# Kernel optimization log

Measured on AMD Instinct MI355X. Metric: run time of the kernel, lower is better.

The kernel has to match this reference:

```python
import jax, jax.numpy as jnp
import numpy as np

N_NODE = 118
DM, DP, DR, DH, DN, DPHI, DE = 768, 128, 128, 256, 256, 192, 256
N_OUT = 2
NEG = -1e9

leaky = lambda z: jnp.where(z >= 0, z, 0.01 * z)


def lstm_layer(x_seq, W_ih, W_hh, b_ih, b_hh):
    # x_seq: [B, T, in]; W_ih: [4H, in]; W_hh: [4H, H]; gate order i,f,g,o (torch)
    B = x_seq.shape[0]
    H = W_hh.shape[1]

    def step(carry, xt):
        h, c = carry
        gates = xt @ W_ih.T + h @ W_hh.T + b_ih + b_hh  # [B, 4H]
        i, f, g, o = jnp.split(gates, 4, axis=1)
        c = jax.nn.sigmoid(f) * c + jax.nn.sigmoid(i) * jnp.tanh(g)
        h = jax.nn.sigmoid(o) * jnp.tanh(c)
        return (h, c), h

    h0 = jnp.zeros((B, H), x_seq.dtype)
    (_, _), hs = jax.lax.scan(step, (h0, h0), jnp.swapaxes(x_seq, 0, 1))
    return jnp.swapaxes(hs, 0, 1)  # [B, T, H]


def setup_inputs() -> dict:
    key = jax.random.key(0)
    ks = jax.random.split(key, 32)
    n_feat, T = 128, 2048
    sc = 0.05
    inp = {}
    inp["x"] = jax.random.normal(ks[0], (N_NODE, T, n_feat), jnp.float32)
    h_pmt = jax.random.uniform(ks[1], (N_NODE, 2), jnp.float32)
    act = jax.random.randint(ks[2], (N_NODE, 1), 0, 2).astype(jnp.float32)
    inp["x_tag"] = jnp.concatenate([h_pmt, act], axis=1)
    # LSTM params (2 layers, hidden=DP)
    inp["W_ih0"] = jax.random.normal(ks[3], (4 * DP, n_feat), jnp.float32) * sc
    inp["W_hh0"] = jax.random.normal(ks[4], (4 * DP, DP), jnp.float32) * sc
    inp["b_ih0"] = jnp.zeros((4 * DP,), jnp.float32)
    inp["b_hh0"] = jnp.zeros((4 * DP,), jnp.float32)
    inp["W_ih1"] = jax.random.normal(ks[5], (4 * DP, DP), jnp.float32) * sc
    inp["W_hh1"] = jax.random.normal(ks[6], (4 * DP, DP), jnp.float32) * sc
    inp["b_ih1"] = jnp.zeros((4 * DP,), jnp.float32)
    inp["b_hh1"] = jnp.zeros((4 * DP,), jnp.float32)
    inp["pseudo_message"] = jax.random.normal(ks[7], (1, DM), jnp.float32) * sc
    inp["Wum"] = jax.random.normal(ks[8], (DM + 1, DR), jnp.float32) * sc
    inp["Wvm"] = jax.random.normal(ks[9], (DM + 1, DR), jnp.float32) * sc
    inp["Wup"] = jax.random.normal(ks[10], (DP, DR), jnp.float32) * sc
    inp["Wvp"] = jax.random.normal(ks[11], (DP, DR), jnp.float32) * sc
    inp["W_hyb"] = jax.random.normal(ks[12], (3 * DR, DH), jnp.float32) * sc
    inp["b_hyb"] = jnp.zeros((DH,), jnp.float32)
    inp["W_act"] = jax.random.normal(ks[13], (DH + 2, DN), jnp.float32) * sc
    inp["b_act"] = jnp.zeros((DN,), jnp.float32)
    inp["W_inact"] = jax.random.normal(ks[14], (DH, DN), jnp.float32) * sc
    inp["b_inact"] = jnp.zeros((DN,), jnp.float32)
    inp["Wphin"] = jax.random.normal(ks[15], (2 * DN, DPHI), jnp.float32) * sc
    inp["aphi"] = jax.random.normal(ks[16], (DPHI, 1), jnp.float32) * sc
    inp["Won"] = jax.random.normal(ks[17], (2 * DN, DN), jnp.float32) * sc
    inp["Weo"] = jax.random.normal(ks[18], (3 * DN, DE), jnp.float32) * sc
    inp["Wi"] = jax.random.normal(ks[19], (N_NODE, DN + 2 * DE, N_OUT), jnp.float32) * sc
    inp["bi"] = jax.random.normal(ks[20], (N_NODE, N_OUT), jnp.float32) * sc
    return inp


def reference(x, x_tag, W_ih0, W_hh0, b_ih0, b_hh0, W_ih1, W_hh1, b_ih1, b_hh1,
              pseudo_message, Wum, Wvm, Wup, Wvp, W_hyb, b_hyb, W_act, b_act,
              W_inact, b_inact, Wphin, aphi, Won, Weo, Wi, bi):
    N = x.shape[0]
    # --- price embedding: 2-layer LSTM, take last hidden ---
    h1 = lstm_layer(x, W_ih0, W_hh0, b_ih0, b_hh0)
    h2 = lstm_layer(h1, W_ih1, W_hh1, b_ih1, b_hh1)
    p = leaky(h2[:, -1, :])  # [N, DP]

    act = x_tag[:, -1:]                      # [N, 1]
    V1 = x_tag[:, -1] == 0
    V0 = x_tag[:, -1] == 1
    m = jnp.broadcast_to(pseudo_message, (N, DM))
    v_m = leaky(jnp.concatenate([m, act], axis=1) @ Wvm)
    u_p = leaky(p @ Wup)
    h_pmt = x_tag[:, 0:2]
    h_hyb = leaky(jnp.concatenate([u_p, u_p + v_m, v_m], axis=1) @ W_hyb + b_hyb)
    n_act = (jnp.concatenate([h_hyb, h_pmt], axis=1) @ W_act + b_act) * (1.0 - act)
    n_inact = (h_hyb @ W_inact + b_inact) * act
    n = leaky(n_act + n_inact)               # [N, DN]

    # pair[i, j] = cat(n[j], n[i])  (matches unsqueeze(0)/unsqueeze(1) repeat order)
    pair = jnp.concatenate([
        jnp.broadcast_to(n[None, :, :], (N, N, DN)),
        jnp.broadcast_to(n[:, None, :], (N, N, DN)),
    ], axis=-1)                               # [N, N, 2*DN]

    phi = (leaky(pair @ Wphin) @ aphi)[..., 0]  # [N, N]
    mask1 = V1[:, None]
    mask0 = V0[:, None]
    phi1 = jax.nn.softmax(jnp.where(mask1, phi, NEG), axis=0)
    phi0 = jax.nn.softmax(jnp.where(mask0, phi, NEG), axis=0)
    phi_masked = jnp.where(mask1, phi1, jnp.where(mask0, phi0, phi))
    phi_all = jax.nn.softmax(phi, axis=0)
    alpha = jnp.where(jnp.sum(V1) > 0, phi_masked, phi_all)

    e = leaky(pair @ Won)
    e = jnp.concatenate([e, pair], axis=-1) @ Weo  # [N, N, DE]
    alpha1 = (1.0 - act) * alpha              # [N, N]
    alpha0 = act * alpha
    hyper_m1 = leaky(jnp.einsum('nj,njd->nd', alpha1, e))
    hyper_m0 = leaky(jnp.einsum('nj,njd->nd', alpha0, e))
    hyper_m = jnp.concatenate([hyper_m0, hyper_m1], axis=-1)
    output = jnp.concatenate([n, hyper_m], axis=-1)  # [N, DN+2*DE]
    y_hat = jnp.einsum('nd,ndo->no', output, Wi) + bi
    y_hat = jax.nn.softmax(y_hat, axis=1)

    o1 = Wum @ Wvm.T
    o2 = Wup @ Wvp.T
    l_ort = jnp.sqrt(jnp.sum(o1 * o1)) + jnp.sqrt(jnp.sum(o2 * o2))

    # vectorized pairwise cosine similarity * sign product over V1 nodes
    nrm = jnp.maximum(jnp.linalg.norm(n, axis=1), 1e-8)
    n_unit = n / nrm[:, None]
    s = jnp.sign(h_pmt[:, 1] - h_pmt[:, 0]) * V1.astype(n.dtype)
    l_pol = jnp.sum((n_unit @ n_unit.T) * (s[:, None] * s[None, :]))

    return (y_hat, h_pmt, l_ort, l_pol, V1, V0)
```

## Files before the change

### kernel.cpp

```cpp
#include <hip/hip_runtime.h>
#include <cstdint>
#include <cstddef>

#define NNODE 118
#define TSEQ  2048
#define TC    512
#define NCH   4
#define NEGC  -1000000000.0f

typedef __fp16 h2v __attribute__((ext_vector_type(2)));
typedef short short8 __attribute__((ext_vector_type(8)));
typedef float floatx4 __attribute__((ext_vector_type(4)));

__device__ __forceinline__ float leakyf(float x){ return x >= 0.f ? x : 0.01f * x; }
__device__ __forceinline__ float frcp(float x){ return __builtin_amdgcn_rcpf(x); }
__device__ __forceinline__ float sigm(float x){ return frcp(1.f + __expf(-x)); }
__device__ __forceinline__ float tanhfast(float x){ return 1.f - 2.f * frcp(__expf(2.f * x) + 1.f); }

__device__ __forceinline__ unsigned short bf16rne(float x){
  unsigned int u = __builtin_bit_cast(unsigned int, x);
  u = (u + 0x7fffu + ((u >> 16) & 1u)) >> 16;
  return (unsigned short)u;
}

__device__ __forceinline__ float fdot2(h2v a, h2v b, float c){
#if __has_builtin(__builtin_amdgcn_fdot2)
  return __builtin_amdgcn_fdot2(a, b, c, false);
#else
  return c + (float)a.x * (float)b.x + (float)a.y * (float)b.y;
#endif
}
__device__ __forceinline__ h2v bch2(unsigned int u){ return __builtin_bit_cast(h2v, u); }

__device__ float bred_sum(float v, float* buf, int nthr){
  int tid = threadIdx.x;
  buf[tid] = v; __syncthreads();
  for (int s = nthr >> 1; s > 0; s >>= 1){
    if (tid < s) buf[tid] += buf[tid + s];
    __syncthreads();
  }
  float r = buf[0]; __syncthreads(); return r;
}
__device__ float bred_max(float v, float* buf, int nthr){
  int tid = threadIdx.x;
  buf[tid] = v; __syncthreads();
  for (int s = nthr >> 1; s > 0; s >>= 1){
    if (tid < s) buf[tid] = fmaxf(buf[tid], buf[tid + s]);
    __syncthreads();
  }
  float r = buf[0]; __syncthreads(); return r;
}

__global__ void f32_to_bf16_k(const float* __restrict__ in, unsigned short* __restrict__ out, int n){
  int i = blockIdx.x * blockDim.x + threadIdx.x;
  if (i < n) out[i] = bf16rne(in[i]);
}
__global__ void f32_to_f16_k(const float* __restrict__ in, __fp16* __restrict__ out, int n){
  int i = blockIdx.x * blockDim.x + threadIdx.x;
  if (i < n) out[i] = (__fp16)in[i];
}

__global__ __launch_bounds__(256, 4) void pregemm(
    const float* __restrict__ A,
    const unsigned short* __restrict__ Wb,
    __fp16* __restrict__ pre,
    int t0)
{
  const int tid = threadIdx.x, lane = tid & 63, wv = tid >> 6;
  const int blk = blockIdx.x;
  const int n = blk / (TC / 64), tb = blk % (TC / 64);
  const int rbase_pre = n * TC + tb * 64 + wv * 16;
  const size_t rbase_gl = (size_t)n * TSEQ + t0 + tb * 64 + wv * 16;
  const int r16 = lane & 15, kq = lane >> 4;
  __shared__ __fp16 lds[4][16 * 132];

  short8 af[4];
  #pragma unroll
  for (int kt = 0; kt < 4; kt++){
    const float* p = A + (rbase_gl + r16) * 128 + kt * 32 + kq * 8;
    float4 x0 = ((const float4*)p)[0];
    float4 x1 = ((const float4*)p)[1];
    short8 s;
    s[0] = (short)bf16rne(x0.x); s[1] = (short)bf16rne(x0.y);
    s[2] = (short)bf16rne(x0.z); s[3] = (short)bf16rne(x0.w);
    s[4] = (short)bf16rne(x1.x); s[5] = (short)bf16rne(x1.y);
    s[6] = (short)bf16rne(x1.z); s[7] = (short)bf16rne(x1.w);
    af[kt] = s;
  }

  __fp16* lw = &lds[wv][0];
  for (int g8 = 0; g8 < 4; g8++){
    #pragma unroll
    for (int ntc = 0; ntc < 8; ntc++){
      int nt = g8 * 8 + ntc;
      floatx4 acc = {0.f, 0.f, 0.f, 0.f};
      #pragma unroll
      for (int kt = 0; kt < 4; kt++){
        const unsigned short* bp = Wb + (size_t)(nt * 16 + r16) * 128 + kt * 32 + kq * 8;
        short8 bfr = __builtin_bit_cast(short8, *(const uint4*)bp);
        acc = __builtin_amdgcn_mfma_f32_16x16x32_bf16(af[kt], bfr, acc, 0, 0, 0);
      }
      #pragma unroll
      for (int r = 0; r < 4; r++){
        int crow = kq * 4 + r, ccol = ntc * 16 + r16;
        lw[crow * 132 + ccol] = (__fp16)acc[r];
      }
    }
    #pragma unroll
    for (int i = 0; i < 4; i++){
      int r2 = i * 4 + kq, ch = r16;
      uint4 v = *(const uint4*)&lw[r2 * 132 + ch * 8];
      *(uint4*)(pre + ((size_t)(rbase_pre + r2)) * 512 + g8 * 128 + ch * 8) = v;
    }
  }
}

__global__ __launch_bounds__(512, 2) void lstm_split(
    const unsigned int* __restrict__ pre1,
    unsigned int* __restrict__ h1ring,
    const __fp16* __restrict__ Wih1,
    const __fp16* __restrict__ Whh0,
    const __fp16* __restrict__ Whh1,
    const float* __restrict__ b_ih0, const float* __restrict__ b_hh0,
    const float* __restrict__ b_ih1, const float* __restrict__ b_hh1,
    unsigned int* __restrict__ hstate1, float* __restrict__ c1state,
    unsigned int* __restrict__ hstate2, float* __restrict__ c2state,
    float* __restrict__ pout, int c)
{
  const int tid = threadIdx.x, lane = tid & 63, w = tid >> 6;
  if (blockIdx.x < NNODE){
    if (c >= NCH) return;
    const int n = blockIdx.x;
    __shared__ float g1buf[2][512];
    __shared__ unsigned int h1own[8][64];
    __shared__ unsigned int lds_pre[2][16 * 256];

    h2v wh[64];
    {
      const uint4* wp = (const uint4*)(Whh0 + (size_t)tid * 128);
      #pragma unroll
      for (int kk = 0; kk < 16; kk++){
        uint4 v = wp[kk];
        wh[4 * kk + 0] = bch2(v.x); wh[4 * kk + 1] = bch2(v.y);
        wh[4 * kk + 2] = bch2(v.z); wh[4 * kk + 3] = bch2(v.w);
      }
    }
    const float bias = b_ih0[tid] + b_hh0[tid];

    float2 c1; unsigned int hcur;
    if (c == 0){ c1.x = 0.f; c1.y = 0.f; hcur = 0u; }
    else { c1 = ((const float2*)c1state)[n * 64 + lane]; hcur = hstate1[n * 64 + lane]; }
    h1own[w][lane] = hcur;

    const uint4* prow4 = (const uint4*)(pre1 + (size_t)n * TC * 256);
    {
      uint4* dst = (uint4*)&lds_pre[0][0];
      dst[tid] = prow4[tid];
      dst[512 + tid] = prow4[512 + tid];
    }
    unsigned int* hring = h1ring + ((size_t)(c & 1) * NNODE + n) * TC * 64;
    __syncthreads();

    #pragma unroll 1
    for (int p = 0; p < TC + 1; p++){
      if (p >= 1){
        const int rb = (p - 1) & 1;
        float2 gi = *(const float2*)&g1buf[rb][2 * lane];
        float2 gf = *(const float2*)&g1buf[rb][128 + 2 * lane];
        float2 gg = *(const float2*)&g1buf[rb][256 + 2 * lane];
        float2 go = *(const float2*)&g1buf[rb][384 + 2 * lane];
        c1.x = sigm(gf.x) * c1.x + sigm(gi.x) * tanhfast(gg.x);
        c1.y = sigm(gf.y) * c1.y + sigm(gi.y) * tanhfast(gg.y);
        float h0 = sigm(go.x) * tanhfast(c1.x);
        float h1v = sigm(go.y) * tanhfast(c1.y);
        h2v hp; hp.x = (__fp16)h0; hp.y = (__fp16)h1v;
        hcur = __builtin_bit_cast(unsigned int, hp);
        h1own[w][lane] = hcur;
        if (w == 0) hring[(size_t)(p - 1) * 64 + lane] = hcur;
      }
      if (p < TC){
        h2v pp = bch2(lds_pre[(p >> 4) & 1][(p & 15) * 256 + (tid >> 1)]);
        float a0 = bias + (float)((tid & 1) ? pp.y : pp.x);
        float a1 = 0.f, a2 = 0.f, a3 = 0.f;
        const uint4* h4 = (const uint4*)&h1own[w][0];
        #pragma unroll
        for (int k = 0; k < 16; k++){
          uint4 hv = h4[k];
          a0 = fdot2(wh[4 * k + 0], bch2(hv.x), a0);
          a1 = fdot2(wh[4 * k + 1], bch2(hv.y), a1);
          a2 = fdot2(wh[4 * k + 2], bch2(hv.z), a2);
          a3 = fdot2(wh[4 * k + 3], bch2(hv.w), a3);
        }
        g1buf[p & 1][tid] = (a0 + a1) + (a2 + a3);
      }
      if ((p & 15) == 0){
        int bn = (p >> 4) + 1;
        if (bn < TC / 16){
          uint4* dst = (uint4*)&lds_pre[bn & 1][0];
          const uint4* src = prow4 + (size_t)bn * 1024;
          dst[tid] = src[tid];
          dst[512 + tid] = src[512 + tid];
        }
      }
      __syncthreads();
    }
    if (w == 0){
      hstate1[n * 64 + lane] = hcur;
      ((float2*)c1state)[n * 64 + lane] = c1;
    }
  } else {
    if (c < 1) return;
    const int n = blockIdx.x - NNODE;
    __shared__ float g2buf[2][512];
    __shared__ unsigned int h2own[8][64];
    __shared__ unsigned int lds_h1[2][16 * 64];

    h2v w1r[64], w2r[64];
    {
      const uint4* wa = (const uint4*)(Wih1 + (size_t)tid * 128);
      const uint4* wb = (const uint4*)(Whh1 + (size_t)tid * 128);
      #pragma unroll
      for (int kk = 0; kk < 16; kk++){
        uint4 v = wa[kk];
        w1r[4 * kk + 0] = bch2(v.x); w1r[4 * kk + 1] = bch2(v.y);
        w1r[4 * kk + 2] = bch2(v.z); w1r[4 * kk + 3] = bch2(v.w);
      }
      #pragma unroll
      for (int kk = 0; kk < 16; kk++){
        uint4 v = wb[kk];
        w2r[4 * kk + 0] = bch2(v.x); w2r[4 * kk + 1] = bch2(v.y);
        w2r[4 * kk + 2] = bch2(v.z); w2r[4 * kk + 3] = bch2(v.w);
      }
    }
    const float bias = b_ih1[tid] + b_hh1[tid];

    float2 c2; unsigned int hcur;
    if (c == 1){ c2.x = 0.f; c2.y = 0.f; hcur = 0u; }
    else { c2 = ((const float2*)c2state)[n * 64 + lane]; hcur = hstate2[n * 64 + lane]; }
    h2own[w][lane] = hcur;

    const uint4* h1src = (const uint4*)(h1ring + ((size_t)((c - 1) & 1) * NNODE + n) * TC * 64);
    if (tid < 256) ((uint4*)&lds_h1[0][0])[tid] = h1src[tid];
    __syncthreads();

    #pragma unroll 1
    for (int p = 0; p < TC + 1; p++){
      if (p >= 1){
        const int rb = (p - 1) & 1;
        float2 gi = *(const float2*)&g2buf[rb][2 * lane];
        float2 gf = *(const float2*)&g2buf[rb][128 + 2 * lane];
        float2 gg = *(const float2*)&g2buf[rb][256 + 2 * lane];
        float2 go = *(const float2*)&g2buf[rb][384 + 2 * lane];
        c2.x = sigm(gf.x) * c2.x + sigm(gi.x) * tanhfast(gg.x);
        c2.y = sigm(gf.y) * c2.y + sigm(gi.y) * tanhfast(gg.y);
        float h0 = sigm(go.x) * tanhfast(c2.x);
        float h1v = sigm(go.y) * tanhfast(c2.y);
        h2v hp; hp.x = (__fp16)h0; hp.y = (__fp16)h1v;
        hcur = __builtin_bit_cast(unsigned int, hp);
        h2own[w][lane] = hcur;
      }
      if (p < TC){
        float a0 = bias, a1 = 0.f, a2 = 0.f, a3 = 0.f;
        const uint4* hh1 = (const uint4*)&lds_h1[(p >> 4) & 1][(p & 15) * 64];
        #pragma unroll
        for (int k = 0; k < 16; k++){
          uint4 hv = hh1[k];
          a0 = fdot2(w1r[4 * k + 0], bch2(hv.x), a0);
          a1 = fdot2(w1r[4 * k + 1], bch2(hv.y), a1);
          a2 = fdot2(w1r[4 * k + 2], bch2(hv.z), a2);
          a3 = fdot2(w1r[4 * k + 3], bch2(hv.w), a3);
        }
        const uint4* hh2 = (const uint4*)&h2own[w][0];
        #pragma unroll
        for (int k = 0; k < 16; k++){
          uint4 hv = hh2[k];
          a0 = fdot2(w2r[4 * k + 0], bch2(hv.x), a0);
          a1 = fdot2(w2r[4 * k + 1], bch2(hv.y), a1);
          a2 = fdot2(w2r[4 * k + 2], bch2(hv.z), a2);
          a3 = fdot2(w2r[4 * k + 3], bch2(hv.w), a3);
        }
        g2buf[p & 1][tid] = (a0 + a1) + (a2 + a3);
      }
      if ((p & 15) == 0){
        int bn = (p >> 4) + 1;
        if (bn < TC / 16 && tid < 256)
          ((uint4*)&lds_h1[bn & 1][0])[tid] = h1src[(size_t)bn * 256 + tid];
      }
      __syncthreads();
    }
    if (w == 0){
      hstate2[n * 64 + lane] = hcur;
      ((float2*)c2state)[n * 64 + lane] = c2;
      if (c == NCH){
        h2v hp = bch2(hcur);
        float2 pv2; pv2.x = leakyf((float)hp.x); pv2.y = leakyf((float)hp.y);
        ((float2*)pout)[n * 64 + lane] = pv2;
      }
    }
  }
}

__global__ void node_mlp(
    const float* __restrict__ x_tag, const float* __restrict__ pm,
    const float* __restrict__ Wvm, const float* __restrict__ Wup,
    const float* __restrict__ W_hyb, const float* __restrict__ b_hyb,
    const float* __restrict__ W_act, const float* __restrict__ b_act,
    const float* __restrict__ W_inact, const float* __restrict__ b_inact,
    const float* __restrict__ p, float* __restrict__ nmat)
{
  int n = blockIdx.x, tid = threadIdx.x;
  __shared__ float pl[128], up[128], vm[128], hh[256];
  float act = x_tag[n * 3 + 2], hp0 = x_tag[n * 3 + 0], hp1 = x_tag[n * 3 + 1];
  if (tid < 128) pl[tid] = p[n * 128 + tid];
  __syncthreads();
  if (tid < 128){
    float a1 = 0.f;
    for (int k = 0; k < 768; k++) a1 += pm[k] * Wvm[k * 128 + tid];
    a1 += act * Wvm[768 * 128 + tid];
    vm[tid] = leakyf(a1);
    float a2 = 0.f;
    for (int k = 0; k < 128; k++) a2 += pl[k] * Wup[k * 128 + tid];
    up[tid] = leakyf(a2);
  }
  __syncthreads();
  {
    float a = b_hyb[tid];
    for (int k = 0; k < 128; k++) a += up[k] * W_hyb[k * 256 + tid];
    for (int k = 0; k < 128; k++) a += (up[k] + vm[k]) * W_hyb[(128 + k) * 256 + tid];
    for (int k = 0; k < 128; k++) a += vm[k] * W_hyb[(256 + k) * 256 + tid];
    hh[tid] = leakyf(a);
  }
  __syncthreads();
  {
    float na = b_act[tid];
    for (int k = 0; k < 256; k++) na += hh[k] * W_act[k * 256 + tid];
    na += hp0 * W_act[256 * 256 + tid] + hp1 * W_act[257 * 256 + tid];
    float ni = b_inact[tid];
    for (int k = 0; k < 256; k++) ni += hh[k] * W_inact[k * 256 + tid];
    nmat[n * 256 + tid] = leakyf(na * (1.f - act) + ni * act);
  }
}

__global__ void node_proj(
    const float* __restrict__ nmat,
    const float* __restrict__ Wphin, const float* __restrict__ Won,
    const float* __restrict__ Weo,
    float* __restrict__ A, float* __restrict__ B,
    float* __restrict__ C, float* __restrict__ D,
    float* __restrict__ Q, float* __restrict__ R)
{
  int n = blockIdx.x, tid = threadIdx.x;
  __shared__ float nl[256];
  nl[tid] = nmat[n * 256 + tid];
  __syncthreads();
  if (tid < 192){
    float a = 0.f, b = 0.f;
    for (int k = 0; k < 256; k++){ float v = nl[k]; a += v * Wphin[k * 192 + tid]; b += v * Wphin[(256 + k) * 192 + tid]; }
    A[n * 192 + tid] = a; B[n * 192 + tid] = b;
  }
  float c = 0.f, d = 0.f, q = 0.f, r = 0.f;
  for (int k = 0; k < 256; k++){
    float v = nl[k];
    c += v * Won[k * 256 + tid];
    d += v * Won[(256 + k) * 256 + tid];
    q += v * Weo[(256 + k) * 256 + tid];
    r += v * Weo[(512 + k) * 256 + tid];
  }
  C[n * 256 + tid] = c; D[n * 256 + tid] = d;
  Q[n * 256 + tid] = q; R[n * 256 + tid] = r;
}

__global__ void phi_kernel(const float* __restrict__ A, const float* __restrict__ B,
                           const float* __restrict__ aphi, float* __restrict__ phiT)
{
  int j = blockIdx.x, tid = threadIdx.x;
  __shared__ float Aj[192], ap[192];
  for (int k = tid; k < 192; k += 128){ Aj[k] = A[j * 192 + k]; ap[k] = aphi[k]; }
  __syncthreads();
  if (tid < NNODE){
    const float* Bi = B + (size_t)tid * 192;
    float s = 0.f;
    for (int k = 0; k < 192; k++) s += leakyf(Aj[k] + Bi[k]) * ap[k];
    phiT[j * NNODE + tid] = s;
  }
}

__global__ void alpha_kernel(const float* __restrict__ phiT, const float* __restrict__ x_tag,
                             float* __restrict__ alpha)
{
  int j = blockIdx.x, tid = threadIdx.x;
  __shared__ float buf[128];
  bool valid = tid < NNODE;
  float ph = valid ? phiT[j * NNODE + tid] : 0.f;
  float a  = valid ? x_tag[tid * 3 + 2] : -1.f;
  bool v1 = (a == 0.f), v0 = (a == 1.f);

  float c1 = bred_sum((valid && v1) ? 1.f : 0.f, buf, 128);

  float x1 = (valid && v1) ? ph : NEGC;
  float m1 = bred_max(valid ? x1 : -3.4e38f, buf, 128);
  float e1 = valid ? __expf(x1 - m1) : 0.f;
  float s1 = bred_sum(e1, buf, 128);
  float p1 = e1 / s1;

  float x0 = (valid && v0) ? ph : NEGC;
  float m0 = bred_max(valid ? x0 : -3.4e38f, buf, 128);
  float e0 = valid ? __expf(x0 - m0) : 0.f;
  float s0 = bred_sum(e0, buf, 128);
  float p0 = e0 / s0;

  float ma = bred_max(valid ? ph : -3.4e38f, buf, 128);
  float ea = valid ? __expf(ph - ma) : 0.f;
  float sa = bred_sum(ea, buf, 128);
  float pa = ea / sa;

  float pmask = v1 ? p1 : (v0 ? p0 : ph);
  float al = (c1 > 0.f) ? pmask : pa;
  if (valid) alpha[tid * NNODE + j] = al;
}

__global__ void att_sum(const float* __restrict__ alpha, const float* __restrict__ C,
                        const float* __restrict__ D, const float* __restrict__ Q,
                        const float* __restrict__ R, const float* __restrict__ nmat,
                        float* __restrict__ T1, float* __restrict__ Spart,
                        float* __restrict__ nrm)
{
  int i = blockIdx.x, tid = threadIdx.x;
  __shared__ float al[128];
  __shared__ float rb[256];
  if (tid < 128) al[tid] = (tid < NNODE) ? alpha[i * NNODE + tid] : 0.f;
  __syncthreads();
  float Di = D[i * 256 + tid];
  float acc1 = 0.f, acc2 = 0.f, sa = 0.f;
  for (int jj = 0; jj < NNODE; jj++){
    float av = al[jj]; sa += av;
    acc1 += av * leakyf(C[jj * 256 + tid] + Di);
    acc2 += av * Q[jj * 256 + tid];
  }
  T1[i * 256 + tid] = acc1;
  Spart[i * 256 + tid] = acc2 + sa * R[i * 256 + tid];
  float nv = nmat[i * 256 + tid];
  float ss = bred_sum(nv * nv, rb, 256);
  if (tid == 0) nrm[i] = fmaxf(sqrtf(ss), 1e-8f);
}

__global__ void finalize_node(const float* __restrict__ T1, const float* __restrict__ Spart,
                              const float* __restrict__ Weo, const float* __restrict__ nmat,
                              const float* __restrict__ x_tag, const float* __restrict__ Wi,
                              const float* __restrict__ bi, const float* __restrict__ nrm,
                              float* __restrict__ vvec, float* __restrict__ out)
{
  int i = blockIdx.x, tid = threadIdx.x;
  __shared__ float t1[256];
  __shared__ float rb[256];
  t1[tid] = T1[i * 256 + tid];
  __syncthreads();
  float s = Spart[i * 256 + tid];
  for (int k = 0; k < 256; k++) s += t1[k] * Weo[k * 256 + tid];
  float act = x_tag[i * 3 + 2], hp0 = x_tag[i * 3 + 0], hp1 = x_tag[i * 3 + 1];
  float hm0 = leakyf(act * s);
  float hm1 = leakyf((1.f - act) * s);
  float nd = nmat[i * 256 + tid];
  const float* Wir = Wi + (size_t)i * 1536;
  float y0 = nd * Wir[tid * 2]     + hm0 * Wir[(256 + tid) * 2]     + hm1 * Wir[(512 + tid) * 2];
  float y1 = nd * Wir[tid * 2 + 1] + hm0 * Wir[(256 + tid) * 2 + 1] + hm1 * Wir[(512 + tid) * 2 + 1];
  y0 = bred_sum(y0, rb, 256);
  y1 = bred_sum(y1, rb, 256);
  float sgn = (hp1 > hp0) ? 1.f : ((hp1 < hp0) ? -1.f : 0.f);
  if (act == 0.f && sgn != 0.f) atomicAdd(vvec + tid, sgn * nd / nrm[i]);
  if (tid == 0){
    y0 += bi[i * 2]; y1 += bi[i * 2 + 1];
    float m = fmaxf(y0, y1);
    float ee0 = __expf(y0 - m), ee1 = __expf(y1 - m);
    float ssum = ee0 + ee1;
    out[i * 2]     = ee0 / ssum;
    out[i * 2 + 1] = ee1 / ssum;
    out[236 + i * 2]     = hp0;
    out[236 + i * 2 + 1] = hp1;
    out[474 + i] = (act == 0.f) ? 1.f : 0.f;
    out[592 + i] = (act == 1.f) ? 1.f : 0.f;
  }
}

__global__ void ort_kernel(const float* __restrict__ Wum, const float* __restrict__ Wvm,
                           const float* __restrict__ Wup, const float* __restrict__ Wvp,
                           float* __restrict__ misc)
{
  int a = blockIdx.x, b = threadIdx.x;
  float g1 = 0.f, g2 = 0.f, g3 = 0.f, g4 = 0.f;
  for (int r = 0; r < 769; r++){
    g1 += Wum[r * 128 + a] * Wum[r * 128 + b];
    g2 += Wvm[r * 128 + a] * Wvm[r * 128 + b];
  }
  for (int r = 0; r < 128; r++){
    g3 += Wup[r * 128 + a] * Wup[r * 128 + b];
    g4 += Wvp[r * 128 + a] * Wvp[r * 128 + b];
  }
  __shared__ float rb[128];
  float s1 = bred_sum(g1 * g2, rb, 128);
  float s2 = bred_sum(g3 * g4, rb, 128);
  if (b == 0){ atomicAdd(misc + 0, s1); atomicAdd(misc + 1, s2); }
}

__global__ void finalize_scalars(const float* __restrict__ misc, const float* __restrict__ vvec,
                                 float* __restrict__ out)
{
  __shared__ float rb[256];
  int tid = threadIdx.x;
  float v = vvec[tid];
  float ss = bred_sum(v * v, rb, 256);
  if (tid == 0){
    out[472] = sqrtf(misc[0]) + sqrtf(misc[1]);
    out[473] = ss;
  }
}

extern "C" void kernel_launch(void* const* d_in, const int* in_sizes, int n_in,
                              void* d_out, int out_size, void* d_ws, size_t ws_size,
                              hipStream_t stream)
{
  const float* x        = (const float*)d_in[0];
  const float* x_tag    = (const float*)d_in[1];
  const float* W_ih0    = (const float*)d_in[2];
  const float* W_hh0    = (const float*)d_in[3];
  const float* b_ih0    = (const float*)d_in[4];
  const float* b_hh0    = (const float*)d_in[5];
  const float* W_ih1    = (const float*)d_in[6];
  const float* W_hh1    = (const float*)d_in[7];
  const float* b_ih1    = (const float*)d_in[8];
  const float* b_hh1    = (const float*)d_in[9];
  const float* pm       = (const float*)d_in[10];
  const float* Wum      = (const float*)d_in[11];
  const float* Wvm      = (const float*)d_in[12];
  const float* Wup      = (const float*)d_in[13];
  const float* Wvp      = (const float*)d_in[14];
  const float* W_hyb    = (const float*)d_in[15];
  const float* b_hyb    = (const float*)d_in[16];
  const float* W_act    = (const float*)d_in[17];
  const float* b_act    = (const float*)d_in[18];
  const float* W_inact  = (const float*)d_in[19];
  const float* b_inact  = (const float*)d_in[20];
  const float* Wphin    = (const float*)d_in[21];
  const float* aphi     = (const float*)d_in[22];
  const float* Won      = (const float*)d_in[23];
  const float* Weo      = (const float*)d_in[24];
  const float* Wi       = (const float*)d_in[25];
  const float* bi       = (const float*)d_in[26];
  float* out = (float*)d_out;

  char* base = (char*)d_ws;
  size_t off = 0;
  auto take = [&](size_t bytes) -> char* {
    char* p = base + off;
    off += (bytes + 255) & ~(size_t)255;
    return p;
  };
  __fp16* pre          = (__fp16*)take((size_t)NNODE * TC * 512 * 2);
  unsigned int* h1ring = (unsigned int*)take((size_t)2 * NNODE * TC * 64 * 4);
  unsigned short* wf0  = (unsigned short*)take((size_t)512 * 128 * 2);
  __fp16* wih1h        = (__fp16*)take((size_t)512 * 128 * 2);
  __fp16* whh0h        = (__fp16*)take((size_t)512 * 128 * 2);
  __fp16* whh1h        = (__fp16*)take((size_t)512 * 128 * 2);
  unsigned int* hs1    = (unsigned int*)take((size_t)NNODE * 64 * 4);
  float* c1s           = (float*)take((size_t)NNODE * 128 * 4);
  unsigned int* hs2    = (unsigned int*)take((size_t)NNODE * 64 * 4);
  float* c2s           = (float*)take((size_t)NNODE * 128 * 4);
  float* pbuf  = (float*)take((size_t)NNODE * 128 * 4);
  float* nmat  = (float*)take((size_t)NNODE * 256 * 4);
  float* Amat  = (float*)take((size_t)NNODE * 192 * 4);
  float* Bmat  = (float*)take((size_t)NNODE * 192 * 4);
  float* Cmat  = (float*)take((size_t)NNODE * 256 * 4);
  float* Dmat  = (float*)take((size_t)NNODE * 256 * 4);
  float* Qmat  = (float*)take((size_t)NNODE * 256 * 4);
  float* Rmat  = (float*)take((size_t)NNODE * 256 * 4);
  float* phiT  = (float*)take((size_t)NNODE * NNODE * 4);
  float* alpha = (float*)take((size_t)NNODE * NNODE * 4);
  float* T1    = (float*)take((size_t)NNODE * 256 * 4);
  float* Spart = (float*)take((size_t)NNODE * 256 * 4);
  float* nrm   = (float*)take((size_t)NNODE * 4);
  float* vvec  = (float*)take(256 * 4);
  float* misc  = (float*)take(8 * 4);

  hipMemsetAsync(vvec, 0, 1024 + 32, stream);

  f32_to_bf16_k<<<256, 256, 0, stream>>>(W_ih0, wf0, 512 * 128);
  f32_to_f16_k<<<256, 256, 0, stream>>>(W_ih1, wih1h, 512 * 128);
  f32_to_f16_k<<<256, 256, 0, stream>>>(W_hh0, whh0h, 512 * 128);
  f32_to_f16_k<<<256, 256, 0, stream>>>(W_hh1, whh1h, 512 * 128);

  const int gemm_grid = NNODE * (TC / 64);
  for (int c = 0; c <= NCH; c++){
    if (c < NCH) pregemm<<<gemm_grid, 256, 0, stream>>>(x, wf0, pre, c * TC);
    lstm_split<<<2 * NNODE, 512, 0, stream>>>((const unsigned int*)pre, h1ring,
                                              wih1h, whh0h, whh1h,
                                              b_ih0, b_hh0, b_ih1, b_hh1,
                                              hs1, c1s, hs2, c2s, pbuf, c);
  }

  node_mlp<<<NNODE, 256, 0, stream>>>(x_tag, pm, Wvm, Wup, W_hyb, b_hyb,
                                      W_act, b_act, W_inact, b_inact, pbuf, nmat);
  node_proj<<<NNODE, 256, 0, stream>>>(nmat, Wphin, Won, Weo, Amat, Bmat, Cmat, Dmat, Qmat, Rmat);
  phi_kernel<<<NNODE, 128, 0, stream>>>(Amat, Bmat, aphi, phiT);
  alpha_kernel<<<NNODE, 128, 0, stream>>>(phiT, x_tag, alpha);
  att_sum<<<NNODE, 256, 0, stream>>>(alpha, Cmat, Dmat, Qmat, Rmat, nmat, T1, Spart, nrm);
  finalize_node<<<NNODE, 256, 0, stream>>>(T1, Spart, Weo, nmat, x_tag, Wi, bi, nrm, vvec, out);
  ort_kernel<<<128, 128, 0, stream>>>(Wum, Wvm, Wup, Wvp, misc);
  finalize_scalars<<<1, 256, 0, stream>>>(misc, vvec, out);
}
```

Measured before the change: 3.499 ms.

## Batch 16 nodes per block and run LSTM recurrences with MFMA

Replaces the per-node dot-product LSTM (one block per node, fdot2 on register weights) with 16 blocks that each own 16 nodes and compute both input and recurrent projections via f16 MFMA each timestep, keeping the weights in registers. The separate bf16 pre-GEMM pass is removed: x is converted once to a swizzled f16 node-major-per-timestep layout and streamed through an LDS ring. This turns the serial recurrence into batched matrix ops over far fewer blocks, trading wide parallelism across CUs for denser per-step compute. It also changes input precision from bf16 to f16.

Result: slower. 5.200 ms (+48.6%).

```diff
diff --git a/kernel.cpp b/kernel.cpp
--- a/kernel.cpp
+++ b/kernel.cpp
@@ -6,10 +6,10 @@
 #define TSEQ  2048
 #define TC    512
 #define NCH   4
+#define BQ    8
 #define NEGC  -1000000000.0f
 
-typedef __fp16 h2v __attribute__((ext_vector_type(2)));
-typedef short short8 __attribute__((ext_vector_type(8)));
+typedef __fp16 f16x8 __attribute__((ext_vector_type(8)));
 typedef float floatx4 __attribute__((ext_vector_type(4)));
 
 __device__ __forceinline__ float leakyf(float x){ return x >= 0.f ? x : 0.01f * x; }
@@ -17,20 +17,9 @@
 __device__ __forceinline__ float sigm(float x){ return frcp(1.f + __expf(-x)); }
 __device__ __forceinline__ float tanhfast(float x){ return 1.f - 2.f * frcp(__expf(2.f * x) + 1.f); }
 
-__device__ __forceinline__ unsigned short bf16rne(float x){
-  unsigned int u = __builtin_bit_cast(unsigned int, x);
-  u = (u + 0x7fffu + ((u >> 16) & 1u)) >> 16;
-  return (unsigned short)u;
-}
-
-__device__ __forceinline__ float fdot2(h2v a, h2v b, float c){
-#if __has_builtin(__builtin_amdgcn_fdot2)
-  return __builtin_amdgcn_fdot2(a, b, c, false);
-#else
-  return c + (float)a.x * (float)b.x + (float)a.y * (float)b.y;
-#endif
-}
-__device__ __forceinline__ h2v bch2(unsigned int u){ return __builtin_bit_cast(h2v, u); }
+__device__ __forceinline__ int swzb(int row, int colByte){
+  return row * 256 + (colByte ^ ((row & 7) << 4));
+}
 
 __device__ float bred_sum(float v, float* buf, int nthr){
   int tid = threadIdx.x;
@@ -51,253 +40,206 @@
   float r = buf[0]; __syncthreads(); return r;
 }
 
-__global__ void f32_to_bf16_k(const float* __restrict__ in, unsigned short* __restrict__ out, int n){
-  int i = blockIdx.x * blockDim.x + threadIdx.x;
-  if (i < n) out[i] = bf16rne(in[i]);
-}
 __global__ void f32_to_f16_k(const float* __restrict__ in, __fp16* __restrict__ out, int n){
   int i = blockIdx.x * blockDim.x + threadIdx.x;
   if (i < n) out[i] = (__fp16)in[i];
 }
 
-__global__ __launch_bounds__(256, 4) void pregemm(
-    const float* __restrict__ A,
-    const unsigned short* __restrict__ Wb,
-    __fp16* __restrict__ pre,
-    int t0)
-{
-  const int tid = threadIdx.x, lane = tid & 63, wv = tid >> 6;
-  const int blk = blockIdx.x;
-  const int n = blk / (TC / 64), tb = blk % (TC / 64);
-  const int rbase_pre = n * TC + tb * 64 + wv * 16;
-  const size_t rbase_gl = (size_t)n * TSEQ + t0 + tb * 64 + wv * 16;
-  const int r16 = lane & 15, kq = lane >> 4;
-  __shared__ __fp16 lds[4][16 * 132];
-
-  short8 af[4];
+__global__ __launch_bounds__(512) void xconv(const float* __restrict__ x, __fp16* __restrict__ xb){
+  const int t = blockIdx.x, tid = threadIdx.x;
+  const int node = tid >> 2, kq = tid & 3;
+  const int k0 = kq * 32;
+  uint4 o[4];
+  if (node < NNODE){
+    const float* src = x + ((size_t)node * TSEQ + t) * 128 + k0;
+    __fp16 tmp[32];
+    #pragma unroll
+    for (int i = 0; i < 8; i++){
+      float4 v = ((const float4*)src)[i];
+      tmp[4*i+0] = (__fp16)v.x; tmp[4*i+1] = (__fp16)v.y;
+      tmp[4*i+2] = (__fp16)v.z; tmp[4*i+3] = (__fp16)v.w;
+    }
+    #pragma unroll
+    for (int i = 0; i < 4; i++) o[i] = ((const uint4*)tmp)[i];
+  } else {
+    #pragma unroll
+    for (int i = 0; i < 4; i++){ o[i].x = 0; o[i].y = 0; o[i].z = 0; o[i].w = 0; }
+  }
+  char* dst = (char*)xb + (size_t)t * 32768 + node * 256;
   #pragma unroll
-  for (int kt = 0; kt < 4; kt++){
-    const float* p = A + (rbase_gl + r16) * 128 + kt * 32 + kq * 8;
-    float4 x0 = ((const float4*)p)[0];
-    float4 x1 = ((const float4*)p)[1];
-    short8 s;
-    s[0] = (short)bf16rne(x0.x); s[1] = (short)bf16rne(x0.y);
-    s[2] = (short)bf16rne(x0.z); s[3] = (short)bf16rne(x0.w);
-    s[4] = (short)bf16rne(x1.x); s[5] = (short)bf16rne(x1.y);
-    s[6] = (short)bf16rne(x1.z); s[7] = (short)bf16rne(x1.w);
-    af[kt] = s;
-  }
-
-  __fp16* lw = &lds[wv][0];
-  for (int g8 = 0; g8 < 4; g8++){
-    #pragma unroll
-    for (int ntc = 0; ntc < 8; ntc++){
-      int nt = g8 * 8 + ntc;
-      floatx4 acc = {0.f, 0.f, 0.f, 0.f};
-      #pragma unroll
-      for (int kt = 0; kt < 4; kt++){
-        const unsigned short* bp = Wb + (size_t)(nt * 16 + r16) * 128 + kt * 32 + kq * 8;
-        short8 bfr = __builtin_bit_cast(short8, *(const uint4*)bp);
-        acc = __builtin_amdgcn_mfma_f32_16x16x32_bf16(af[kt], bfr, acc, 0, 0, 0);
-      }
-      #pragma unroll
-      for (int r = 0; r < 4; r++){
-        int crow = kq * 4 + r, ccol = ntc * 16 + r16;
-        lw[crow * 132 + ccol] = (__fp16)acc[r];
-      }
-    }
-    #pragma unroll
-    for (int i = 0; i < 4; i++){
-      int r2 = i * 4 + kq, ch = r16;
-      uint4 v = *(const uint4*)&lw[r2 * 132 + ch * 8];
-      *(uint4*)(pre + ((size_t)(rbase_pre + r2)) * 512 + g8 * 128 + ch * 8) = v;
-    }
-  }
-}
-
-__global__ __launch_bounds__(512, 2) void lstm_split(
-    const unsigned int* __restrict__ pre1,
-    unsigned int* __restrict__ h1ring,
-    const __fp16* __restrict__ Wih1,
-    const __fp16* __restrict__ Whh0,
-    const __fp16* __restrict__ Whh1,
+  for (int i = 0; i < 4; i++){
+    int cb = (k0 * 2 + i * 16) ^ ((node & 7) << 4);
+    *(uint4*)(dst + cb) = o[i];
+  }
+}
+
+__global__ __launch_bounds__(256)
+__attribute__((amdgpu_waves_per_eu(1, 1)))
+void lstm_mfma(
+    const __fp16* __restrict__ xb,
+    __fp16* __restrict__ h1ring,
+    const __fp16* __restrict__ Wih0h, const __fp16* __restrict__ Whh0h,
+    const __fp16* __restrict__ Wih1h, const __fp16* __restrict__ Whh1h,
     const float* __restrict__ b_ih0, const float* __restrict__ b_hh0,
     const float* __restrict__ b_ih1, const float* __restrict__ b_hh1,
-    unsigned int* __restrict__ hstate1, float* __restrict__ c1state,
-    unsigned int* __restrict__ hstate2, float* __restrict__ c2state,
+    __fp16* __restrict__ hstate1, float* __restrict__ c1state,
+    __fp16* __restrict__ hstate2, float* __restrict__ c2state,
     float* __restrict__ pout, int c)
 {
-  const int tid = threadIdx.x, lane = tid & 63, w = tid >> 6;
-  if (blockIdx.x < NNODE){
-    if (c >= NCH) return;
-    const int n = blockIdx.x;
-    __shared__ float g1buf[2][512];
-    __shared__ unsigned int h1own[8][64];
-    __shared__ unsigned int lds_pre[2][16 * 256];
-
-    h2v wh[64];
-    {
-      const uint4* wp = (const uint4*)(Whh0 + (size_t)tid * 128);
-      #pragma unroll
-      for (int kk = 0; kk < 16; kk++){
-        uint4 v = wp[kk];
-        wh[4 * kk + 0] = bch2(v.x); wh[4 * kk + 1] = bch2(v.y);
-        wh[4 * kk + 2] = bch2(v.z); wh[4 * kk + 3] = bch2(v.w);
+  __shared__ __fp16 ring[2][BQ][2048];
+  __shared__ __fp16 hbuf[2][2048];
+  __shared__ uint4 lds_pad[768];
+
+  const int tid = threadIdx.x;
+  if (blockIdx.x == 0x7fffffffu) lds_pad[tid].x = tid;
+
+  const bool isL1 = blockIdx.x < 8;
+  if (isL1){ if (c >= NCH) return; } else { if (c < 1) return; }
+
+  const int n0 = (blockIdx.x & 7) * 16;
+  const int w = tid >> 6, lane = tid & 63;
+  const int q = lane >> 4, l16 = lane & 15;
+
+  const __fp16* WAsrc = isL1 ? Wih0h : Wih1h;
+  const __fp16* WBsrc = isL1 ? Whh0h : Whh1h;
+  const float*  bia   = isL1 ? b_ih0 : b_ih1;
+  const float*  bib   = isL1 ? b_hh0 : b_hh1;
+  __fp16* hst = isL1 ? hstate1 : hstate2;
+  float*  cst = isL1 ? c1state : c2state;
+  const bool zinit = isL1 ? (c == 0) : (c == 1);
+  const __fp16* sb = isL1 ? (xb + (size_t)(c * TC) * 16384 + (size_t)n0 * 128)
+                          : (h1ring + (size_t)(((c - 1) & 1) * TC) * 16384 + (size_t)n0 * 128);
+  char* ringw = (char*)(h1ring + (size_t)((c & 1) * TC) * 16384) + n0 * 256;
+
+  f16x8 WA[2][4][4], WB[2][4][4];
+  #pragma unroll
+  for (int dg = 0; dg < 2; dg++)
+    #pragma unroll
+    for (int g = 0; g < 4; g++){
+      const int gate = g * 128 + dg * 64 + w * 16 + l16;
+      const __fp16* wa = WAsrc + (size_t)gate * 128 + q * 8;
+      const __fp16* wb = WBsrc + (size_t)gate * 128 + q * 8;
+      #pragma unroll
+      for (int kt = 0; kt < 4; kt++){
+        WA[dg][g][kt] = *(const f16x8*)(wa + kt * 32);
+        WB[dg][g][kt] = *(const f16x8*)(wb + kt * 32);
       }
     }
-    const float bias = b_ih0[tid] + b_hh0[tid];
-
-    float2 c1; unsigned int hcur;
-    if (c == 0){ c1.x = 0.f; c1.y = 0.f; hcur = 0u; }
-    else { c1 = ((const float2*)c1state)[n * 64 + lane]; hcur = hstate1[n * 64 + lane]; }
-    h1own[w][lane] = hcur;
-
-    const uint4* prow4 = (const uint4*)(pre1 + (size_t)n * TC * 256);
-    {
-      uint4* dst = (uint4*)&lds_pre[0][0];
-      dst[tid] = prow4[tid];
-      dst[512 + tid] = prow4[512 + tid];
-    }
-    unsigned int* hring = h1ring + ((size_t)(c & 1) * NNODE + n) * TC * 64;
+  float bias[2][4];
+  #pragma unroll
+  for (int dg = 0; dg < 2; dg++)
+    #pragma unroll
+    for (int g = 0; g < 4; g++){
+      const int gi = g * 128 + dg * 64 + w * 16 + l16;
+      bias[dg][g] = bia[gi] + bib[gi];
+    }
+
+  float creg[2][4];
+  __fp16 hv[2][4];
+  #pragma unroll
+  for (int dg = 0; dg < 2; dg++)
+    #pragma unroll
+    for (int r = 0; r < 4; r++){
+      const int node = q * 4 + r;
+      const int d = dg * 64 + w * 16 + l16;
+      __fp16 h0;
+      if (zinit){ creg[dg][r] = 0.f; h0 = (__fp16)0.f; }
+      else { creg[dg][r] = cst[(size_t)(n0 + node) * 128 + d]; h0 = hst[(size_t)(n0 + node) * 128 + d]; }
+      *(__fp16*)((char*)&hbuf[1][0] + swzb(node, 2 * d)) = h0;
+    }
+
+  #pragma unroll
+  for (int hh = 0; hh < 2; hh++){
+    const int t = hh * 4 + w;
+    const uint4* s = (const uint4*)((const char*)(sb + (size_t)t * 16384) + lane * 64);
+    uint4* d = (uint4*)((char*)&ring[0][t][0] + lane * 64);
+    #pragma unroll
+    for (int i = 0; i < 4; i++) d[i] = s[i];
+  }
+  __syncthreads();
+
+  uint4 sreg[4];
+
+  #pragma unroll 1
+  for (int p = 0; p < TC; p++){
+    const char* xt = (const char*)&ring[(p >> 3) & 1][p & 7][0];
+    const char* ht = (const char*)&hbuf[(p & 1) ^ 1][0];
+    f16x8 ax[4], ah[4];
+    #pragma unroll
+    for (int kt = 0; kt < 4; kt++){
+      const int off = swzb(l16, kt * 64 + q * 16);
+      ax[kt] = *(const f16x8*)(xt + off);
+      ah[kt] = *(const f16x8*)(ht + off);
+    }
+    floatx4 acc[2][4];
+    #pragma unroll
+    for (int dg = 0; dg < 2; dg++)
+      #pragma unroll
+      for (int g = 0; g < 4; g++){ acc[dg][g].x = 0.f; acc[dg][g].y = 0.f; acc[dg][g].z = 0.f; acc[dg][g].w = 0.f; }
+    #pragma unroll
+    for (int kt = 0; kt < 4; kt++){
+      #pragma unroll
+      for (int dg = 0; dg < 2; dg++)
+        #pragma unroll
+        for (int g = 0; g < 4; g++){
+          acc[dg][g] = __builtin_amdgcn_mfma_f32_16x16x32_f16(ax[kt], WA[dg][g][kt], acc[dg][g], 0, 0, 0);
+          acc[dg][g] = __builtin_amdgcn_mfma_f32_16x16x32_f16(ah[kt], WB[dg][g][kt], acc[dg][g], 0, 0, 0);
+        }
+    }
+    char* hb = (char*)&hbuf[p & 1][0];
+    #pragma unroll
+    for (int dg = 0; dg < 2; dg++)
+      #pragma unroll
+      for (int r = 0; r < 4; r++){
+        const float gi = acc[dg][0][r] + bias[dg][0];
+        const float gf = acc[dg][1][r] + bias[dg][1];
+        const float gg = acc[dg][2][r] + bias[dg][2];
+        const float go = acc[dg][3][r] + bias[dg][3];
+        float cc = creg[dg][r];
+        cc = sigm(gf) * cc + sigm(gi) * tanhfast(gg);
+        creg[dg][r] = cc;
+        const float h = sigm(go) * tanhfast(cc);
+        hv[dg][r] = (__fp16)h;
+        const int node = q * 4 + r;
+        const int off = swzb(node, 2 * (dg * 64 + w * 16 + l16));
+        *(__fp16*)(hb + off) = hv[dg][r];
+        if (isL1) *(__fp16*)(ringw + (size_t)p * 32768 + off) = hv[dg][r];
+      }
+    const int kn = (p >> 3) + 1;
+    const bool sv = kn < (TC / BQ);
+    const int ph = p & 7;
+    if (ph == 0 && sv){
+      const uint4* s = (const uint4*)((const char*)(sb + (size_t)(kn * BQ + w) * 16384) + lane * 64);
+      #pragma unroll
+      for (int i = 0; i < 4; i++) sreg[i] = s[i];
+    } else if (ph == 2 && sv){
+      uint4* d = (uint4*)((char*)&ring[kn & 1][w][0] + lane * 64);
+      #pragma unroll
+      for (int i = 0; i < 4; i++) d[i] = sreg[i];
+    } else if (ph == 4 && sv){
+      const uint4* s = (const uint4*)((const char*)(sb + (size_t)(kn * BQ + 4 + w) * 16384) + lane * 64);
+      #pragma unroll
+      for (int i = 0; i < 4; i++) sreg[i] = s[i];
+    } else if (ph == 6 && sv){
+      uint4* d = (uint4*)((char*)&ring[kn & 1][4 + w][0] + lane * 64);
+      #pragma unroll
+      for (int i = 0; i < 4; i++) d[i] = sreg[i];
+    }
     __syncthreads();
-
-    #pragma unroll 1
-    for (int p = 0; p < TC + 1; p++){
-      if (p >= 1){
-        const int rb = (p - 1) & 1;
-        float2 gi = *(const float2*)&g1buf[rb][2 * lane];
-        float2 gf = *(const float2*)&g1buf[rb][128 + 2 * lane];
-        float2 gg = *(const float2*)&g1buf[rb][256 + 2 * lane];
-        float2 go = *(const float2*)&g1buf[rb][384 + 2 * lane];
-        c1.x = sigm(gf.x) * c1.x + sigm(gi.x) * tanhfast(gg.x);
-        c1.y = sigm(gf.y) * c1.y + sigm(gi.y) * tanhfast(gg.y);
-        float h0 = sigm(go.x) * tanhfast(c1.x);
-        float h1v = sigm(go.y) * tanhfast(c1.y);
-        h2v hp; hp.x = (__fp16)h0; hp.y = (__fp16)h1v;
-        hcur = __builtin_bit_cast(unsigned int, hp);
-        h1own[w][lane] = hcur;
-        if (w == 0) hring[(size_t)(p - 1) * 64 + lane] = hcur;
-      }
-      if (p < TC){
-        h2v pp = bch2(lds_pre[(p >> 4) & 1][(p & 15) * 256 + (tid >> 1)]);
-        float a0 = bias + (float)((tid & 1) ? pp.y : pp.x);
-        float a1 = 0.f, a2 = 0.f, a3 = 0.f;
-        const uint4* h4 = (const uint4*)&h1own[w][0];
-        #pragma unroll
-        for (int k = 0; k < 16; k++){
-          uint4 hv = h4[k];
-          a0 = fdot2(wh[4 * k + 0], bch2(hv.x), a0);
-          a1 = fdot2(wh[4 * k + 1], bch2(hv.y), a1);
-          a2 = fdot2(wh[4 * k + 2], bch2(hv.z), a2);
-          a3 = fdot2(wh[4 * k + 3], bch2(hv.w), a3);
-        }
-        g1buf[p & 1][tid] = (a0 + a1) + (a2 + a3);
-      }
-      if ((p & 15) == 0){
-        int bn = (p >> 4) + 1;
-        if (bn < TC / 16){
-          uint4* dst = (uint4*)&lds_pre[bn & 1][0];
-          const uint4* src = prow4 + (size_t)bn * 1024;
-          dst[tid] = src[tid];
-          dst[512 + tid] = src[512 + tid];
-        }
-      }
-      __syncthreads();
-    }
-    if (w == 0){
-      hstate1[n * 64 + lane] = hcur;
-      ((float2*)c1state)[n * 64 + lane] = c1;
-    }
-  } else {
-    if (c < 1) return;
-    const int n = blockIdx.x - NNODE;
-    __shared__ float g2buf[2][512];
-    __shared__ unsigned int h2own[8][64];
-    __shared__ unsigned int lds_h1[2][16 * 64];
-
-    h2v w1r[64], w2r[64];
-    {
-      const uint4* wa = (const uint4*)(Wih1 + (size_t)tid * 128);
-      const uint4* wb = (const uint4*)(Whh1 + (size_t)tid * 128);
-      #pragma unroll
-      for (int kk = 0; kk < 16; kk++){
-        uint4 v = wa[kk];
-        w1r[4 * kk + 0] = bch2(v.x); w1r[4 * kk + 1] = bch2(v.y);
-        w1r[4 * kk + 2] = bch2(v.z); w1r[4 * kk + 3] = bch2(v.w);
-      }
-      #pragma unroll
-      for (int kk = 0; kk < 16; kk++){
-        uint4 v = wb[kk];
-        w2r[4 * kk + 0] = bch2(v.x); w2r[4 * kk + 1] = bch2(v.y);
-        w2r[4 * kk + 2] = bch2(v.z); w2r[4 * kk + 3] = bch2(v.w);
-      }
-    }
-    const float bias = b_ih1[tid] + b_hh1[tid];
-
-    float2 c2; unsigned int hcur;
-    if (c == 1){ c2.x = 0.f; c2.y = 0.f; hcur = 0u; }
-    else { c2 = ((const float2*)c2state)[n * 64 + lane]; hcur = hstate2[n * 64 + lane]; }
-    h2own[w][lane] = hcur;
-
-    const uint4* h1src = (const uint4*)(h1ring + ((size_t)((c - 1) & 1) * NNODE + n) * TC * 64);
-    if (tid < 256) ((uint4*)&lds_h1[0][0])[tid] = h1src[tid];
-    __syncthreads();
-
-    #pragma unroll 1
-    for (int p = 0; p < TC + 1; p++){
-      if (p >= 1){
-        const int rb = (p - 1) & 1;
-        float2 gi = *(const float2*)&g2buf[rb][2 * lane];
-        float2 gf = *(const float2*)&g2buf[rb][128 + 2 * lane];
-        float2 gg = *(const float2*)&g2buf[rb][256 + 2 * lane];
-        float2 go = *(const float2*)&g2buf[rb][384 + 2 * lane];
-        c2.x = sigm(gf.x) * c2.x + sigm(gi.x) * tanhfast(gg.x);
-        c2.y = sigm(gf.y) * c2.y + sigm(gi.y) * tanhfast(gg.y);
-        float h0 = sigm(go.x) * tanhfast(c2.x);
-        float h1v = sigm(go.y) * tanhfast(c2.y);
-        h2v hp; hp.x = (__fp16)h0; hp.y = (__fp16)h1v;
-        hcur = __builtin_bit_cast(unsigned int, hp);
-        h2own[w][lane] = hcur;
-      }
-      if (p < TC){
-        float a0 = bias, a1 = 0.f, a2 = 0.f, a3 = 0.f;
-        const uint4* hh1 = (const uint4*)&lds_h1[(p >> 4) & 1][(p & 15) * 64];
-        #pragma unroll
-        for (int k = 0; k < 16; k++){
-          uint4 hv = hh1[k];
-          a0 = fdot2(w1r[4 * k + 0], bch2(hv.x), a0);
-          a1 = fdot2(w1r[4 * k + 1], bch2(hv.y), a1);
-          a2 = fdot2(w1r[4 * k + 2], bch2(hv.z), a2);
-          a3 = fdot2(w1r[4 * k + 3], bch2(hv.w), a3);
-        }
-        const uint4* hh2 = (const uint4*)&h2own[w][0];
-        #pragma unroll
-        for (int k = 0; k < 16; k++){
-          uint4 hv = hh2[k];
-          a0 = fdot2(w2r[4 * k + 0], bch2(hv.x), a0);
-          a1 = fdot2(w2r[4 * k + 1], bch2(hv.y), a1);
-          a2 = fdot2(w2r[4 * k + 2], bch2(hv.z), a2);
-          a3 = fdot2(w2r[4 * k + 3], bch2(hv.w), a3);
-        }
-        g2buf[p & 1][tid] = (a0 + a1) + (a2 + a3);
-      }
-      if ((p & 15) == 0){
-        int bn = (p >> 4) + 1;
-        if (bn < TC / 16 && tid < 256)
-          ((uint4*)&lds_h1[bn & 1][0])[tid] = h1src[(size_t)bn * 256 + tid];
-      }
-      __syncthreads();
-    }
-    if (w == 0){
-      hstate2[n * 64 + lane] = hcur;
-      ((float2*)c2state)[n * 64 + lane] = c2;
-      if (c == NCH){
-        h2v hp = bch2(hcur);
-        float2 pv2; pv2.x = leakyf((float)hp.x); pv2.y = leakyf((float)hp.y);
-        ((float2*)pout)[n * 64 + lane] = pv2;
-      }
-    }
-  }
+  }
+
+  #pragma unroll
+  for (int dg = 0; dg < 2; dg++)
+    #pragma unroll
+    for (int r = 0; r < 4; r++){
+      const int node = q * 4 + r;
+      const int d = dg * 64 + w * 16 + l16;
+      const size_t idx = (size_t)(n0 + node) * 128 + d;
+      cst[idx] = creg[dg][r];
+      hst[idx] = hv[dg][r];
+      if (!isL1 && c == NCH && (n0 + node) < NNODE)
+        pout[idx] = leakyf((float)hv[dg][r]);
+    }
 }
 
 __global__ void node_mlp(
@@ -555,16 +497,16 @@
     off += (bytes + 255) & ~(size_t)255;
     return p;
   };
-  __fp16* pre          = (__fp16*)take((size_t)NNODE * TC * 512 * 2);
-  unsigned int* h1ring = (unsigned int*)take((size_t)2 * NNODE * TC * 64 * 4);
-  unsigned short* wf0  = (unsigned short*)take((size_t)512 * 128 * 2);
-  __fp16* wih1h        = (__fp16*)take((size_t)512 * 128 * 2);
-  __fp16* whh0h        = (__fp16*)take((size_t)512 * 128 * 2);
-  __fp16* whh1h        = (__fp16*)take((size_t)512 * 128 * 2);
-  unsigned int* hs1    = (unsigned int*)take((size_t)NNODE * 64 * 4);
-  float* c1s           = (float*)take((size_t)NNODE * 128 * 4);
-  unsigned int* hs2    = (unsigned int*)take((size_t)NNODE * 64 * 4);
-  float* c2s           = (float*)take((size_t)NNODE * 128 * 4);
+  __fp16* xbuf   = (__fp16*)take((size_t)TSEQ * 128 * 128 * 2);
+  __fp16* h1ring = (__fp16*)take((size_t)2 * TC * 128 * 128 * 2);
+  __fp16* wih0h  = (__fp16*)take((size_t)512 * 128 * 2);
+  __fp16* wih1h  = (__fp16*)take((size_t)512 * 128 * 2);
+  __fp16* whh0h  = (__fp16*)take((size_t)512 * 128 * 2);
+  __fp16* whh1h  = (__fp16*)take((size_t)512 * 128 * 2);
+  __fp16* hs1    = (__fp16*)take((size_t)128 * 128 * 2);
+  float* c1s     = (float*)take((size_t)128 * 128 * 4);
+  __fp16* hs2    = (__fp16*)take((size_t)128 * 128 * 2);
+  float* c2s     = (float*)take((size_t)128 * 128 * 4);
   float* pbuf  = (float*)take((size_t)NNODE * 128 * 4);
   float* nmat  = (float*)take((size_t)NNODE * 256 * 4);
   float* Amat  = (float*)take((size_t)NNODE * 192 * 4);
@@ -583,18 +525,17 @@
 
   hipMemsetAsync(vvec, 0, 1024 + 32, stream);
 
-  f32_to_bf16_k<<<256, 256, 0, stream>>>(W_ih0, wf0, 512 * 128);
+  f32_to_f16_k<<<256, 256, 0, stream>>>(W_ih0, wih0h, 512 * 128);
   f32_to_f16_k<<<256, 256, 0, stream>>>(W_ih1, wih1h, 512 * 128);
   f32_to_f16_k<<<256, 256, 0, stream>>>(W_hh0, whh0h, 512 * 128);
   f32_to_f16_k<<<256, 256, 0, stream>>>(W_hh1, whh1h, 512 * 128);
-
-  const int gemm_grid = NNODE * (TC / 64);
+  xconv<<<TSEQ, 512, 0, stream>>>(x, xbuf);
+
   for (int c = 0; c <= NCH; c++){
-    if (c < NCH) pregemm<<<gemm_grid, 256, 0, stream>>>(x, wf0, pre, c * TC);
-    lstm_split<<<2 * NNODE, 512, 0, stream>>>((const unsigned int*)pre, h1ring,
-                                              wih1h, whh0h, whh1h,
-                                              b_ih0, b_hh0, b_ih1, b_hh1,
-                                              hs1, c1s, hs2, c2s, pbuf, c);
+    lstm_mfma<<<16, 256, 0, stream>>>(xbuf, h1ring,
+                                      wih0h, whh0h, wih1h, whh1h,
+                                      b_ih0, b_hh0, b_ih1, b_hh1,
+                                      hs1, c1s, hs2, c2s, pbuf, c);
   }
 
   node_mlp<<<NNODE, 256, 0, stream>>>(x_tag, pm, Wvm, Wup, W_hyb, b_hyb,
```
